# Optimization experiments

Measured on AMD Instinct MI355X. Metric: run time of the kernel, lower is better.

## Reference

```python
import jax, jax.numpy as jnp
import numpy as np

NUM_EXPERTS = 64
TOP_K = 2


def setup_inputs() -> dict:
    key = jax.random.key(0)
    k1, k2 = jax.random.split(key)
    B, D, E = 16384, 4096, NUM_EXPERTS
    routing_features = jax.random.normal(k1, (B, D), dtype=jnp.float32)
    # nn.Linear(D, E, bias=False) weight: [E, D], kaiming-uniform-ish init
    bound = 1.0 / np.sqrt(D)
    gate_w = jax.random.uniform(k2, (E, D), dtype=jnp.float32, minval=-bound, maxval=bound)
    return {"routing_features": routing_features, "gate_w": gate_w}


def reference(routing_features, gate_w):
    B = routing_features.shape[0]
    E, K = NUM_EXPERTS, TOP_K
    # linear gate (no bias): [B, E]
    logits = jnp.einsum("bd,ed->be", routing_features, gate_w)
    full_probs = jax.nn.softmax(logits, axis=-1)
    top_k_logits, top_k_indices = jax.lax.top_k(logits, K)  # [B, K]
    top_k_weights = jax.nn.softmax(top_k_logits, axis=-1)
    # load-balance loss: f_i = fraction of (token, slot) assignments to expert i
    tokens_per_expert = jnp.zeros((E,), dtype=jnp.float32).at[top_k_indices.reshape(-1)].add(1.0)
    f = tokens_per_expert / (B * K)
    P = full_probs.mean(axis=0)
    aux_loss = E * jnp.sum(f * P)
    return top_k_weights, top_k_indices, aux_loss
```

## Files before the change

kernel.cpp:

```cpp
#include <hip/hip_runtime.h>
#include <math.h>


typedef __attribute__((ext_vector_type(8))) short bf16x8;
typedef __attribute__((ext_vector_type(4))) float f32x4;

constexpr int B_ROWS  = 16384;
constexpr int D_DIM   = 4096;
constexpr int E_EXP   = 64;
constexpr int NTHR    = 512;
constexpr int TM      = 128;
constexpr int KSEG    = 256;
constexpr int NSPLIT  = D_DIM / KSEG;
constexpr int NS      = KSEG / 32;
constexpr int FLAGCAP = 8192;
constexpr float GAPTHR = 1e-3f;

__device__ __forceinline__ float wave_max64(float v) {
#pragma unroll
  for (int m = 32; m >= 1; m >>= 1) v = fmaxf(v, __shfl_xor(v, m, 64));
  return v;
}
__device__ __forceinline__ float wave_sum64(float v) {
#pragma unroll
  for (int m = 32; m >= 1; m >>= 1) v += __shfl_xor(v, m, 64);
  return v;
}
__device__ __forceinline__ void wave_argmax64(float v, int i, float& mv, int& mi) {
#pragma unroll
  for (int m = 32; m >= 1; m >>= 1) {
    float ov = __shfl_xor(v, m, 64);
    int   oi = __shfl_xor(i, m, 64);
    if (ov > v || (ov == v && oi < i)) { v = ov; i = oi; }
  }
  mv = v; mi = i;
}

__device__ __forceinline__ void async_copy16(void* lds_dst, const void* g_src) {
  auto g = (const __attribute__((address_space(1))) char*)(g_src);
  auto l = (__attribute__((address_space(3))) char*)(lds_dst);
  __builtin_amdgcn_global_load_lds(g, l, 16, 0, 0);
}

__device__ __forceinline__ void split8(const f32x4 a, const f32x4 b, bf16x8& hi, bf16x8& lo) {
  float f[8] = {a[0], a[1], a[2], a[3], b[0], b[1], b[2], b[3]};
#pragma unroll
  for (int i = 0; i < 8; ++i) {
    unsigned int u = __float_as_uint(f[i]);
    hi[i] = (short)(u >> 16);
    float rem = f[i] - __uint_as_float(u & 0xffff0000u);
    lo[i] = (short)(__float_as_uint(rem) >> 16);
  }
}

__global__ __launch_bounds__(NTHR) void wsplit(const float* __restrict__ gw,
                                               char* __restrict__ wsW,
                                               unsigned int* __restrict__ hdr) {
  const int n = blockIdx.x;
  const int t = threadIdx.x;
  if (n == 0 && t < 192) hdr[t] = 0u;
  const int lane = t & 63, h = (t >> 6) & 1, wc = t >> 7;
  const int col = wc * 16 + (lane & 15);
  const int k0  = n * 32 + (lane >> 4) * 8;
  const float* src = gw + (size_t)col * D_DIM + k0;
  union { unsigned short us[8]; uint4 v; } pk;
#pragma unroll
  for (int i = 0; i < 8; ++i) {
    float f = src[i];
    unsigned int u = __float_as_uint(f);
    if (h == 0) {
      pk.us[i] = (unsigned short)(u >> 16);
    } else {
      float rem = f - __uint_as_float(u & 0xffff0000u);
      pk.us[i] = (unsigned short)(__float_as_uint(rem) >> 16);
    }
  }
  *(uint4*)(wsW + (size_t)n * 8192 + (size_t)t * 16) = pk.v;
}

__global__ __launch_bounds__(NTHR) void gemm_partial(
    const float* __restrict__ rf, const char* __restrict__ wsW,
    float* __restrict__ part) {
  __shared__ char wlds[NS * 8192] __attribute__((aligned(16)));

  const int t = threadIdx.x, lane = t & 63, wv = t >> 6;
  const int ks   = blockIdx.x >> 7;
  const int rb   = blockIdx.x & 127;
  const int row0 = rb * TM;

  {
    const char* src = wsW + (size_t)ks * (NS * 8192);
#pragma unroll
    for (int i = 0; i < NS; ++i)
      async_copy16(wlds + i * 8192 + t * 16, src + i * 8192 + t * 16);
  }
  __syncthreads();

  const float* aptr = rf + (size_t)(row0 + wv * 16 + (lane & 15)) * D_DIM
                         + ks * KSEG + (lane >> 4) * 8;

  f32x4 acc[4] = {{0.f,0.f,0.f,0.f},{0.f,0.f,0.f,0.f},{0.f,0.f,0.f,0.f},{0.f,0.f,0.f,0.f}};
  f32x4 a0[4], a1[4];

#define LDA(s, n) { a0[s] = *(const f32x4*)(aptr + (n) * 32); \
                    a1[s] = *(const f32x4*)(aptr + (n) * 32 + 4); }

  LDA(0, 0); LDA(1, 1); LDA(2, 2); LDA(3, 3);
  __builtin_amdgcn_sched_barrier(0);

#pragma unroll
  for (int n = 0; n < NS; ++n) {
    const int s = n & 3;
    bf16x8 ahi, alo;
    split8(a0[s], a1[s], ahi, alo);
    if (n + 4 < NS) LDA(s, n + 4);
    __builtin_amdgcn_sched_barrier(0);
    const char* wn = wlds + n * 8192 + lane * 16;
#pragma unroll
    for (int cb = 0; cb < 4; ++cb) {
      bf16x8 whi = *(const bf16x8*)(wn + cb * 2048);
      bf16x8 wlo = *(const bf16x8*)(wn + cb * 2048 + 1024);
      acc[cb] = __builtin_amdgcn_mfma_f32_16x16x32_bf16(ahi, whi, acc[cb], 0, 0, 0);
      acc[cb] = __builtin_amdgcn_mfma_f32_16x16x32_bf16(alo, whi, acc[cb], 0, 0, 0);
      acc[cb] = __builtin_amdgcn_mfma_f32_16x16x32_bf16(ahi, wlo, acc[cb], 0, 0, 0);
    }
    __builtin_amdgcn_sched_barrier(0);
  }
#undef LDA

  const int colb = lane & 15;
  const int rowb = (lane >> 4) * 4;
  float* dst = part + ((size_t)ks * B_ROWS + row0 + wv * 16 + rowb) * E_EXP + colb;
#pragma unroll
  for (int cb = 0; cb < 4; ++cb)
#pragma unroll
    for (int j = 0; j < 4; ++j)
      dst[(size_t)j * E_EXP + cb * 16] = acc[cb][j];
}

__global__ __launch_bounds__(NTHR) void epilogue(
    const float* __restrict__ part, float* __restrict__ out,
    float* __restrict__ psum, unsigned int* __restrict__ cnt,
    int* __restrict__ flagcnt, int* __restrict__ flaglist) {
  __shared__ float pcol[E_EXP];
  __shared__ unsigned int scnt[E_EXP];

  const int t = threadIdx.x, lane = t & 63, wv = t >> 6;
  const int row0 = blockIdx.x * 64;

  if (t < E_EXP) { scnt[t] = 0; pcol[t] = 0.f; }
  __syncthreads();

#pragma unroll
  for (int j = 0; j < 8; ++j) {
    const int row = row0 + wv * 8 + j;
    float lg = 0.f;
#pragma unroll
    for (int s = 0; s < NSPLIT; ++s)
      lg += part[((size_t)s * B_ROWS + row) * E_EXP + lane];

    const float m  = wave_max64(lg);
    const float p  = __expf(lg - m);
    const float ss = wave_sum64(p);
    atomicAdd(&pcol[lane], p / ss);

    float v1; int i1; wave_argmax64(lg, lane, v1, i1);
    const float lm1 = (lane == i1) ? -INFINITY : lg;
    float v2; int i2; wave_argmax64(lm1, lane, v2, i2);
    const float lm2 = (lane == i2) ? -INFINITY : lm1;
    float v3; int i3; wave_argmax64(lm2, lane, v3, i3);
    if (lane == 0) {
      const float ex = expf(v2 - v1);
      out[row * 2 + 0] = 1.f / (1.f + ex);
      out[row * 2 + 1] = ex / (1.f + ex);
      out[2 * B_ROWS + row * 2 + 0] = (float)i1;
      out[2 * B_ROWS + row * 2 + 1] = (float)i2;
      atomicAdd(&scnt[i1], 1u);
      atomicAdd(&scnt[i2], 1u);
      if (v1 - v2 < GAPTHR || v2 - v3 < GAPTHR) {
        int fi = atomicAdd(flagcnt, 1);
        if (fi < FLAGCAP) flaglist[fi] = row;
      }
    }
  }
  __syncthreads();
  if (t < E_EXP) {
    atomicAdd(&psum[t], pcol[t]);
    const unsigned int c = scnt[t];
    if (c) atomicAdd(&cnt[t], c);
  }
}

__global__ __launch_bounds__(256) void cleanup(
    const float* __restrict__ rf, const float* __restrict__ gw,
    const int* __restrict__ flagcnt, const int* __restrict__ flaglist,
    const float* __restrict__ psum, const unsigned int* __restrict__ cnt,
    float* __restrict__ out) {
  __shared__ double sm[256];
  const int t = threadIdx.x;
  if (blockIdx.x == 0 && t < 64) {
    const float f = (float)cnt[t] / (float)(B_ROWS * 2);
    const float P = psum[t] / (float)B_ROWS;
    float v = wave_sum64(f * P);
    if (t == 0) out[4 * B_ROWS] = (float)E_EXP * v;
  }
  const int nf = min(*flagcnt, FLAGCAP);
  for (int fi = blockIdx.x; fi < nf; fi += gridDim.x) {
    const int row = flaglist[fi];
    const int e = t & 63, seg = t >> 6;
    const float* a = rf + (size_t)row * D_DIM + seg * 1024;
    const float* w = gw + (size_t)e * D_DIM + seg * 1024;
    double p0 = 0.0, p1 = 0.0, p2 = 0.0, p3 = 0.0;
    for (int k = 0; k < 1024; k += 4) {
      p0 = fma((double)a[k + 0], (double)w[k + 0], p0);
      p1 = fma((double)a[k + 1], (double)w[k + 1], p1);
      p2 = fma((double)a[k + 2], (double)w[k + 2], p2);
      p3 = fma((double)a[k + 3], (double)w[k + 3], p3);
    }
    sm[t] = (p0 + p1) + (p2 + p3);
    __syncthreads();
    if (t < 64) {
      const double l = sm[t] + sm[64 + t] + sm[128 + t] + sm[192 + t];
      double v = l; int ii = t;
#pragma unroll
      for (int m = 32; m >= 1; m >>= 1) {
        double ov = __shfl_xor(v, m, 64); int oi = __shfl_xor(ii, m, 64);
        if (ov > v || (ov == v && oi < ii)) { v = ov; ii = oi; }
      }
      const double v1 = v; const int i1 = ii;
      const double lm = (t == i1) ? -1e300 : l;
      v = lm; ii = t;
#pragma unroll
      for (int m = 32; m >= 1; m >>= 1) {
        double ov = __shfl_xor(v, m, 64); int oi = __shfl_xor(ii, m, 64);
        if (ov > v || (ov == v && oi < ii)) { v = ov; ii = oi; }
      }
      const double v2 = v; const int i2 = ii;
      if (t == 0) {
        const double ex = exp(v2 - v1);
        out[row * 2 + 0] = (float)(1.0 / (1.0 + ex));
        out[row * 2 + 1] = (float)(ex / (1.0 + ex));
        out[2 * B_ROWS + row * 2 + 0] = (float)i1;
        out[2 * B_ROWS + row * 2 + 1] = (float)i2;
      }
    }
    __syncthreads();
  }
}

extern "C" void kernel_launch(void* const* d_in, const int* in_sizes, int n_in,
                              void* d_out, int out_size, void* d_ws, size_t ws_size,
                              hipStream_t stream) {
  const float* rf = (const float*)d_in[0];
  const float* gw = (const float*)d_in[1];
  float* out = (float*)d_out;
  float* psum = (float*)d_ws;
  unsigned int* cnt = (unsigned int*)((char*)d_ws + 256);
  int* flagcnt = (int*)((char*)d_ws + 512);
  int* flaglist = (int*)((char*)d_ws + 768);
  char* wsW = (char*)d_ws + (1u << 20);
  float* part = (float*)((char*)d_ws + (2u << 20));

  wsplit<<<D_DIM / 32, NTHR, 0, stream>>>(gw, wsW, (unsigned int*)d_ws);
  gemm_partial<<<NSPLIT * (B_ROWS / TM), NTHR, 0, stream>>>(rf, wsW, part);
  epilogue<<<B_ROWS / 64, NTHR, 0, stream>>>(part, out, psum, cnt, flagcnt, flaglist);
  cleanup<<<64, 256, 0, stream>>>(rf, gw, flagcnt, flaglist, psum, cnt, out);
}
```

Measured before the change: 237.2 us.

## Double-buffer A and W tiles through LDS with async copies in split-K GEMM

The gate GEMM now streams both the fp32 activation tile (XOR-swizzled) and the split bf16 weights into double-buffered LDS using async copies, overlapping the next stage's loads with the current MFMA work. The K segment per block doubles and the block shrinks to 256 threads, each wave now computing 32 rows with two accumulator sets. This halves the split-K partial output and epilogue reduction traffic and improves reuse of the weight tiles. In exchange each block does longer serial work and synchronizes twice per step, and the manual vmcnt waits must match the copy counts exactly.

```diff
diff --git a/kernel.cpp b/kernel.cpp
--- a/kernel.cpp
+++ b/kernel.cpp
@@ -9,8 +9,9 @@
 constexpr int D_DIM   = 4096;
 constexpr int E_EXP   = 64;
 constexpr int NTHR    = 512;
+constexpr int GTHR    = 256;
 constexpr int TM      = 128;
-constexpr int KSEG    = 256;
+constexpr int KSEG    = 512;
 constexpr int NSPLIT  = D_DIM / KSEG;
 constexpr int NS      = KSEG / 32;
 constexpr int FLAGCAP = 8192;
@@ -78,64 +79,91 @@
   *(uint4*)(wsW + (size_t)n * 8192 + (size_t)t * 16) = pk.v;
 }
 
-__global__ __launch_bounds__(NTHR) void gemm_partial(
+__global__ __launch_bounds__(GTHR) void gemm_partial(
     const float* __restrict__ rf, const char* __restrict__ wsW,
     float* __restrict__ part) {
-  __shared__ char wlds[NS * 8192] __attribute__((aligned(16)));
+  __shared__ char lds[49152] __attribute__((aligned(16)));
 
   const int t = threadIdx.x, lane = t & 63, wv = t >> 6;
-  const int ks   = blockIdx.x >> 7;
-  const int rb   = blockIdx.x & 127;
+  const int rb = blockIdx.x & 127, ks = blockIdx.x >> 7;
   const int row0 = rb * TM;
 
-  {
-    const char* src = wsW + (size_t)ks * (NS * 8192);
-#pragma unroll
-    for (int i = 0; i < NS; ++i)
-      async_copy16(wlds + i * 8192 + t * 16, src + i * 8192 + t * 16);
-  }
-  __syncthreads();
-
-  const float* aptr = rf + (size_t)(row0 + wv * 16 + (lane & 15)) * D_DIM
-                         + ks * KSEG + (lane >> 4) * 8;
-
-  f32x4 acc[4] = {{0.f,0.f,0.f,0.f},{0.f,0.f,0.f,0.f},{0.f,0.f,0.f,0.f},{0.f,0.f,0.f,0.f}};
-  f32x4 a0[4], a1[4];
-
-#define LDA(s, n) { a0[s] = *(const f32x4*)(aptr + (n) * 32); \
-                    a1[s] = *(const f32x4*)(aptr + (n) * 32 + 4); }
-
-  LDA(0, 0); LDA(1, 1); LDA(2, 2); LDA(3, 3);
-  __builtin_amdgcn_sched_barrier(0);
-
-#pragma unroll
+  int goffA[4];
+#pragma unroll
+  for (int j = 0; j < 4; ++j) {
+    const int q = j * GTHR + t;
+    const int row = q >> 3, sl = q & 7;
+    goffA[j] = (row0 + row) * D_DIM + ks * KSEG + ((sl ^ (row & 7)) << 2);
+  }
+  const char* wsrc = wsW + (size_t)(ks * NS) * 8192;
+
+  const int s0 = (lane >> 4) * 2;
+  const int rr0 = wv * 32 + (lane & 15);
+  const int rr1 = rr0 + 16;
+  const int a00 = rr0 * 128 + ((s0 ^ (rr0 & 7)) << 4);
+  const int a01 = rr0 * 128 + (((s0 + 1) ^ (rr0 & 7)) << 4);
+  const int a10 = rr1 * 128 + ((s0 ^ (rr1 & 7)) << 4);
+  const int a11 = rr1 * 128 + (((s0 + 1) ^ (rr1 & 7)) << 4);
+
+  f32x4 acc0[4] = {{0.f,0.f,0.f,0.f},{0.f,0.f,0.f,0.f},{0.f,0.f,0.f,0.f},{0.f,0.f,0.f,0.f}};
+  f32x4 acc1[4] = {{0.f,0.f,0.f,0.f},{0.f,0.f,0.f,0.f},{0.f,0.f,0.f,0.f},{0.f,0.f,0.f,0.f}};
+
+#define ISSUE(n)                                                             \
+  {                                                                          \
+    char* ab_ = lds + ((n) & 1) * 16384;                                     \
+    char* wb_ = lds + 32768 + ((n) & 1) * 8192;                              \
+    _Pragma("unroll") for (int j = 0; j < 4; ++j)                            \
+      async_copy16(ab_ + (j * GTHR + t) * 16, rf + goffA[j] + (n) * 32);     \
+    async_copy16(wb_ + t * 16, wsrc + (size_t)(n) * 8192 + t * 16);          \
+    async_copy16(wb_ + (GTHR + t) * 16,                                      \
+                 wsrc + (size_t)(n) * 8192 + (GTHR + t) * 16);               \
+  }
+
+  ISSUE(0);
+#pragma unroll 2
   for (int n = 0; n < NS; ++n) {
-    const int s = n & 3;
-    bf16x8 ahi, alo;
-    split8(a0[s], a1[s], ahi, alo);
-    if (n + 4 < NS) LDA(s, n + 4);
-    __builtin_amdgcn_sched_barrier(0);
-    const char* wn = wlds + n * 8192 + lane * 16;
+    if (n + 1 < NS) {
+      ISSUE(n + 1);
+      asm volatile("s_waitcnt vmcnt(6)" ::: "memory");
+    } else {
+      asm volatile("s_waitcnt vmcnt(0)" ::: "memory");
+    }
+    __builtin_amdgcn_s_barrier();
+
+    const char* ab = lds + (n & 1) * 16384;
+    const char* wb = lds + 32768 + (n & 1) * 8192 + lane * 16;
+    const f32x4 fl0 = *(const f32x4*)(ab + a00);
+    const f32x4 fh0 = *(const f32x4*)(ab + a01);
+    const f32x4 fl1 = *(const f32x4*)(ab + a10);
+    const f32x4 fh1 = *(const f32x4*)(ab + a11);
+    bf16x8 ahi0, alo0, ahi1, alo1;
+    split8(fl0, fh0, ahi0, alo0);
+    split8(fl1, fh1, ahi1, alo1);
 #pragma unroll
     for (int cb = 0; cb < 4; ++cb) {
-      bf16x8 whi = *(const bf16x8*)(wn + cb * 2048);
-      bf16x8 wlo = *(const bf16x8*)(wn + cb * 2048 + 1024);
-      acc[cb] = __builtin_amdgcn_mfma_f32_16x16x32_bf16(ahi, whi, acc[cb], 0, 0, 0);
-      acc[cb] = __builtin_amdgcn_mfma_f32_16x16x32_bf16(alo, whi, acc[cb], 0, 0, 0);
-      acc[cb] = __builtin_amdgcn_mfma_f32_16x16x32_bf16(ahi, wlo, acc[cb], 0, 0, 0);
-    }
-    __builtin_amdgcn_sched_barrier(0);
-  }
-#undef LDA
+      const bf16x8 whi = *(const bf16x8*)(wb + cb * 2048);
+      const bf16x8 wlo = *(const bf16x8*)(wb + cb * 2048 + 1024);
+      acc0[cb] = __builtin_amdgcn_mfma_f32_16x16x32_bf16(ahi0, whi, acc0[cb], 0, 0, 0);
+      acc0[cb] = __builtin_amdgcn_mfma_f32_16x16x32_bf16(alo0, whi, acc0[cb], 0, 0, 0);
+      acc0[cb] = __builtin_amdgcn_mfma_f32_16x16x32_bf16(ahi0, wlo, acc0[cb], 0, 0, 0);
+      acc1[cb] = __builtin_amdgcn_mfma_f32_16x16x32_bf16(ahi1, whi, acc1[cb], 0, 0, 0);
+      acc1[cb] = __builtin_amdgcn_mfma_f32_16x16x32_bf16(alo1, whi, acc1[cb], 0, 0, 0);
+      acc1[cb] = __builtin_amdgcn_mfma_f32_16x16x32_bf16(ahi1, wlo, acc1[cb], 0, 0, 0);
+    }
+    __builtin_amdgcn_s_barrier();
+  }
+#undef ISSUE
 
   const int colb = lane & 15;
   const int rowb = (lane >> 4) * 4;
-  float* dst = part + ((size_t)ks * B_ROWS + row0 + wv * 16 + rowb) * E_EXP + colb;
+  float* dst = part + ((size_t)ks * B_ROWS + row0 + wv * 32 + rowb) * E_EXP + colb;
 #pragma unroll
   for (int cb = 0; cb < 4; ++cb)
 #pragma unroll
-    for (int j = 0; j < 4; ++j)
-      dst[(size_t)j * E_EXP + cb * 16] = acc[cb][j];
+    for (int j = 0; j < 4; ++j) {
+      dst[(size_t)j * E_EXP + cb * 16] = acc0[cb][j];
+      dst[(size_t)(j + 16) * E_EXP + cb * 16] = acc1[cb][j];
+    }
 }
 
 __global__ __launch_bounds__(NTHR) void epilogue(
@@ -262,7 +290,7 @@
   float* part = (float*)((char*)d_ws + (2u << 20));
 
   wsplit<<<D_DIM / 32, NTHR, 0, stream>>>(gw, wsW, (unsigned int*)d_ws);
-  gemm_partial<<<NSPLIT * (B_ROWS / TM), NTHR, 0, stream>>>(rf, wsW, part);
+  gemm_partial<<<NSPLIT * (B_ROWS / TM), GTHR, 0, stream>>>(rf, wsW, part);
   epilogue<<<B_ROWS / 64, NTHR, 0, stream>>>(part, out, psum, cnt, flagcnt, flaglist);
   cleanup<<<64, 256, 0, stream>>>(rf, gw, flagcnt, flaglist, psum, cnt, out);
 }
```

Result: faster. 204.4 us (-13.8%).

## Stage A and W tiles through triple-buffered LDS with async copies

Applied to the files above, without the earlier changes.

The split-K GEMM now uses 256-thread blocks of 64 rows with 512-wide K segments. Each 32-wide K step of both the activation tile (XOR-swizzled) and the split weight tile is loaded asynchronously into a three-slot LDS ring, with vmcnt waits and barriers keeping two stages in flight. Previously activations were loaded straight from global into registers and all the weights were preloaded up front. This aims to overlap global loads with MFMA work and halve the partial-sum traffic, at the cost of more barriers per step and fewer rows per block.

```diff
diff --git a/kernel.cpp b/kernel.cpp
--- a/kernel.cpp
+++ b/kernel.cpp
@@ -9,8 +9,9 @@
 constexpr int D_DIM   = 4096;
 constexpr int E_EXP   = 64;
 constexpr int NTHR    = 512;
-constexpr int TM      = 128;
-constexpr int KSEG    = 256;
+constexpr int GTHR    = 256;
+constexpr int TM      = 64;
+constexpr int KSEG    = 512;
 constexpr int NSPLIT  = D_DIM / KSEG;
 constexpr int NS      = KSEG / 32;
 constexpr int FLAGCAP = 8192;
@@ -78,55 +79,72 @@
   *(uint4*)(wsW + (size_t)n * 8192 + (size_t)t * 16) = pk.v;
 }
 
-__global__ __launch_bounds__(NTHR) void gemm_partial(
+__global__ __launch_bounds__(GTHR) void gemm_partial(
     const float* __restrict__ rf, const char* __restrict__ wsW,
     float* __restrict__ part) {
-  __shared__ char wlds[NS * 8192] __attribute__((aligned(16)));
+  __shared__ char lds[3 * 16384] __attribute__((aligned(16)));
 
   const int t = threadIdx.x, lane = t & 63, wv = t >> 6;
-  const int ks   = blockIdx.x >> 7;
-  const int rb   = blockIdx.x & 127;
+  const int rb = blockIdx.x & 255, ks = blockIdx.x >> 8;
   const int row0 = rb * TM;
 
-  {
-    const char* src = wsW + (size_t)ks * (NS * 8192);
-#pragma unroll
-    for (int i = 0; i < NS; ++i)
-      async_copy16(wlds + i * 8192 + t * 16, src + i * 8192 + t * 16);
-  }
-  __syncthreads();
-
-  const float* aptr = rf + (size_t)(row0 + wv * 16 + (lane & 15)) * D_DIM
-                         + ks * KSEG + (lane >> 4) * 8;
+  int goffA[2];
+#pragma unroll
+  for (int j = 0; j < 2; ++j) {
+    const int q = j * GTHR + t;
+    const int row = q >> 3, sl = q & 7;
+    goffA[j] = (row0 + row) * D_DIM + ks * KSEG + ((sl ^ (row & 7)) << 2);
+  }
+  const char* wsrc = wsW + (size_t)(ks * NS) * 8192;
+
+  const int rr  = wv * 16 + (lane & 15);
+  const int s0  = (lane >> 4) * 2;
+  const int a00 = rr * 128 + ((s0 ^ (rr & 7)) << 4);
+  const int a01 = rr * 128 + (((s0 + 1) ^ (rr & 7)) << 4);
 
   f32x4 acc[4] = {{0.f,0.f,0.f,0.f},{0.f,0.f,0.f,0.f},{0.f,0.f,0.f,0.f},{0.f,0.f,0.f,0.f}};
-  f32x4 a0[4], a1[4];
-
-#define LDA(s, n) { a0[s] = *(const f32x4*)(aptr + (n) * 32); \
-                    a1[s] = *(const f32x4*)(aptr + (n) * 32 + 4); }
-
-  LDA(0, 0); LDA(1, 1); LDA(2, 2); LDA(3, 3);
-  __builtin_amdgcn_sched_barrier(0);
-
+
+#define ISSUE(nn)                                                            \
+  {                                                                          \
+    char* b_ = lds + ((nn) % 3) * 16384;                                     \
+    async_copy16(b_ + t * 16, rf + goffA[0] + (nn) * 32);                    \
+    async_copy16(b_ + (GTHR + t) * 16, rf + goffA[1] + (nn) * 32);           \
+    async_copy16(b_ + 8192 + t * 16, wsrc + (size_t)(nn) * 8192 + t * 16);   \
+    async_copy16(b_ + 8192 + (GTHR + t) * 16,                                \
+                 wsrc + (size_t)(nn) * 8192 + (GTHR + t) * 16);              \
+  }
+
+  ISSUE(0);
+  ISSUE(1);
 #pragma unroll
   for (int n = 0; n < NS; ++n) {
-    const int s = n & 3;
+    if (n + 2 < NS) {
+      ISSUE(n + 2);
+      asm volatile("s_waitcnt vmcnt(8)" ::: "memory");
+    } else if (n + 1 < NS) {
+      asm volatile("s_waitcnt vmcnt(4)" ::: "memory");
+    } else {
+      asm volatile("s_waitcnt vmcnt(0)" ::: "memory");
+    }
+    __builtin_amdgcn_s_barrier();
+
+    const char* ab = lds + (n % 3) * 16384;
+    const char* wb = ab + 8192 + lane * 16;
+    const f32x4 fl = *(const f32x4*)(ab + a00);
+    const f32x4 fh = *(const f32x4*)(ab + a01);
     bf16x8 ahi, alo;
-    split8(a0[s], a1[s], ahi, alo);
-    if (n + 4 < NS) LDA(s, n + 4);
-    __builtin_amdgcn_sched_barrier(0);
-    const char* wn = wlds + n * 8192 + lane * 16;
+    split8(fl, fh, ahi, alo);
 #pragma unroll
     for (int cb = 0; cb < 4; ++cb) {
-      bf16x8 whi = *(const bf16x8*)(wn + cb * 2048);
-      bf16x8 wlo = *(const bf16x8*)(wn + cb * 2048 + 1024);
+      const bf16x8 whi = *(const bf16x8*)(wb + cb * 2048);
+      const bf16x8 wlo = *(const bf16x8*)(wb + cb * 2048 + 1024);
       acc[cb] = __builtin_amdgcn_mfma_f32_16x16x32_bf16(ahi, whi, acc[cb], 0, 0, 0);
       acc[cb] = __builtin_amdgcn_mfma_f32_16x16x32_bf16(alo, whi, acc[cb], 0, 0, 0);
       acc[cb] = __builtin_amdgcn_mfma_f32_16x16x32_bf16(ahi, wlo, acc[cb], 0, 0, 0);
     }
-    __builtin_amdgcn_sched_barrier(0);
-  }
-#undef LDA
+    __builtin_amdgcn_s_barrier();
+  }
+#undef ISSUE
 
   const int colb = lane & 15;
   const int rowb = (lane >> 4) * 4;
@@ -262,7 +280,7 @@
   float* part = (float*)((char*)d_ws + (2u << 20));
 
   wsplit<<<D_DIM / 32, NTHR, 0, stream>>>(gw, wsW, (unsigned int*)d_ws);
-  gemm_partial<<<NSPLIT * (B_ROWS / TM), NTHR, 0, stream>>>(rf, wsW, part);
+  gemm_partial<<<NSPLIT * (B_ROWS / TM), GTHR, 0, stream>>>(rf, wsW, part);
   epilogue<<<B_ROWS / 64, NTHR, 0, stream>>>(part, out, psum, cnt, flagcnt, flaglist);
   cleanup<<<64, 256, 0, stream>>>(rf, gw, flagcnt, flaglist, psum, cnt, out);
 }
```

New measurement: 210.4 us. 11.3% less time.

## Fuse split-K GEMM and epilogue into single-wave full-K router kernel

Applied to the files above, without the earlier changes.

Replaces the split-K GEMM plus separate epilogue with one kernel where each 64-thread block computes full-K logits for 32 rows. A and W tiles are streamed into a 4-slot LDS ring via async copies with manual vmcnt waits, using an XOR swizzle for A. The softmax, top-k and aux statistics are computed in the same kernel from an LDS tile. This removes the partial-sum buffer write and re-read (16 splits × B×E floats) and one kernel launch. The cost is that each block has only one wave, so latency hiding depends on the async prefetch depth and occupancy, and the weights are re-read from L2 by every block.

```diff
diff --git a/kernel.cpp b/kernel.cpp
--- a/kernel.cpp
+++ b/kernel.cpp
@@ -9,10 +9,9 @@
 constexpr int D_DIM   = 4096;
 constexpr int E_EXP   = 64;
 constexpr int NTHR    = 512;
-constexpr int TM      = 128;
-constexpr int KSEG    = 256;
-constexpr int NSPLIT  = D_DIM / KSEG;
-constexpr int NS      = KSEG / 32;
+constexpr int RPB     = 32;
+constexpr int NS      = 128;
+constexpr int SLOT    = 12288;
 constexpr int FLAGCAP = 8192;
 constexpr float GAPTHR = 1e-3f;
 
@@ -59,10 +58,10 @@
   const int n = blockIdx.x;
   const int t = threadIdx.x;
   if (n == 0 && t < 192) hdr[t] = 0u;
-  const int lane = t & 63, h = (t >> 6) & 1, wc = t >> 7;
-  const int col = wc * 16 + (lane & 15);
-  const int k0  = n * 32 + (lane >> 4) * 8;
-  const float* src = gw + (size_t)col * D_DIM + k0;
+  const int lane = t & 63, h = (t >> 6) & 1, er = t >> 7;
+  const int e  = er * 16 + (lane & 15);
+  const int k0 = n * 32 + (lane >> 4) * 8;
+  const float* src = gw + (size_t)e * D_DIM + k0;
   union { unsigned short us[8]; uint4 v; } pk;
 #pragma unroll
   for (int i = 0; i < 8; ++i) {
@@ -78,117 +77,131 @@
   *(uint4*)(wsW + (size_t)n * 8192 + (size_t)t * 16) = pk.v;
 }
 
-__global__ __launch_bounds__(NTHR) void gemm_partial(
+__global__ __launch_bounds__(64) void gemm_router(
     const float* __restrict__ rf, const char* __restrict__ wsW,
-    float* __restrict__ part) {
-  __shared__ char wlds[NS * 8192] __attribute__((aligned(16)));
-
-  const int t = threadIdx.x, lane = t & 63, wv = t >> 6;
-  const int ks   = blockIdx.x >> 7;
-  const int rb   = blockIdx.x & 127;
-  const int row0 = rb * TM;
-
-  {
-    const char* src = wsW + (size_t)ks * (NS * 8192);
-#pragma unroll
-    for (int i = 0; i < NS; ++i)
-      async_copy16(wlds + i * 8192 + t * 16, src + i * 8192 + t * 16);
-  }
-  __syncthreads();
-
-  const float* aptr = rf + (size_t)(row0 + wv * 16 + (lane & 15)) * D_DIM
-                         + ks * KSEG + (lane >> 4) * 8;
-
-  f32x4 acc[4] = {{0.f,0.f,0.f,0.f},{0.f,0.f,0.f,0.f},{0.f,0.f,0.f,0.f},{0.f,0.f,0.f,0.f}};
-  f32x4 a0[4], a1[4];
-
-#define LDA(s, n) { a0[s] = *(const f32x4*)(aptr + (n) * 32); \
-                    a1[s] = *(const f32x4*)(aptr + (n) * 32 + 4); }
-
-  LDA(0, 0); LDA(1, 1); LDA(2, 2); LDA(3, 3);
-  __builtin_amdgcn_sched_barrier(0);
-
-#pragma unroll
-  for (int n = 0; n < NS; ++n) {
-    const int s = n & 3;
-    bf16x8 ahi, alo;
-    split8(a0[s], a1[s], ahi, alo);
-    if (n + 4 < NS) LDA(s, n + 4);
+    float* __restrict__ out, float* __restrict__ psum,
+    unsigned int* __restrict__ cnt, int* __restrict__ flagcnt,
+    int* __restrict__ flaglist) {
+  __shared__ char lds[4 * SLOT] __attribute__((aligned(16)));
+
+  const int lane = threadIdx.x;
+  const int row0 = blockIdx.x * RPB;
+
+  int goffA[4];
+#pragma unroll
+  for (int j = 0; j < 4; ++j) {
+    const int row = 8 * j + (lane >> 3);
+    const int sl  = lane & 7;
+    goffA[j] = (row0 + row) * D_DIM + ((sl ^ (row & 7)) << 2);
+  }
+
+  const int s0 = (lane >> 4) * 2;
+  int aoff[2][2];
+#pragma unroll
+  for (int rr = 0; rr < 2; ++rr) {
+    const int R = 16 * rr + (lane & 15);
+    aoff[rr][0] = R * 128 + (((s0)     ^ (R & 7)) << 4);
+    aoff[rr][1] = R * 128 + (((s0 + 1) ^ (R & 7)) << 4);
+  }
+
+  f32x4 acc[8] = {{0.f,0.f,0.f,0.f},{0.f,0.f,0.f,0.f},{0.f,0.f,0.f,0.f},{0.f,0.f,0.f,0.f},
+                  {0.f,0.f,0.f,0.f},{0.f,0.f,0.f,0.f},{0.f,0.f,0.f,0.f},{0.f,0.f,0.f,0.f}};
+
+#define ISSUE(nn)                                                             \
+  {                                                                           \
+    char* b_ = lds + ((nn) & 3) * SLOT;                                       \
+    _Pragma("unroll") for (int j = 0; j < 4; ++j)                             \
+      async_copy16(b_ + (j * 64 + lane) * 16, rf + goffA[j] + (nn) * 32);     \
+    _Pragma("unroll") for (int j = 0; j < 8; ++j)                             \
+      async_copy16(b_ + 4096 + (j * 64 + lane) * 16,                          \
+                   wsW + (size_t)(nn) * 8192 + (j * 64 + lane) * 16);         \
+  }
+
+#define STEP(nn)                                                              \
+  {                                                                           \
+    const char* ab = lds + ((nn) & 3) * SLOT;                                 \
+    bf16x8 bhi0, blo0, bhi1, blo1;                                            \
+    {                                                                         \
+      f32x4 fl = *(const f32x4*)(ab + aoff[0][0]);                            \
+      f32x4 fh = *(const f32x4*)(ab + aoff[0][1]);                            \
+      split8(fl, fh, bhi0, blo0);                                             \
+    }                                                                         \
+    {                                                                         \
+      f32x4 fl = *(const f32x4*)(ab + aoff[1][0]);                            \
+      f32x4 fh = *(const f32x4*)(ab + aoff[1][1]);                            \
+      split8(fl, fh, bhi1, blo1);                                             \
+    }                                                                         \
+    _Pragma("unroll") for (int er = 0; er < 4; ++er) {                        \
+      const bf16x8 whi = *(const bf16x8*)(ab + 4096 + er * 2048 + lane * 16); \
+      const bf16x8 wlo = *(const bf16x8*)(ab + 4096 + er * 2048 + 1024 + lane * 16); \
+      acc[er*2+0] = __builtin_amdgcn_mfma_f32_16x16x32_bf16(whi, bhi0, acc[er*2+0], 0, 0, 0); \
+      acc[er*2+0] = __builtin_amdgcn_mfma_f32_16x16x32_bf16(wlo, bhi0, acc[er*2+0], 0, 0, 0); \
+      acc[er*2+0] = __builtin_amdgcn_mfma_f32_16x16x32_bf16(whi, blo0, acc[er*2+0], 0, 0, 0); \
+      acc[er*2+1] = __builtin_amdgcn_mfma_f32_16x16x32_bf16(whi, bhi1, acc[er*2+1], 0, 0, 0); \
+      acc[er*2+1] = __builtin_amdgcn_mfma_f32_16x16x32_bf16(wlo, bhi1, acc[er*2+1], 0, 0, 0); \
+      acc[er*2+1] = __builtin_amdgcn_mfma_f32_16x16x32_bf16(whi, blo1, acc[er*2+1], 0, 0, 0); \
+    }                                                                         \
+  }
+
+  ISSUE(0); ISSUE(1); ISSUE(2);
+  for (int n = 0; n < NS - 3; ++n) {
+    asm volatile("s_waitcnt vmcnt(24)" ::: "memory");
     __builtin_amdgcn_sched_barrier(0);
-    const char* wn = wlds + n * 8192 + lane * 16;
-#pragma unroll
-    for (int cb = 0; cb < 4; ++cb) {
-      bf16x8 whi = *(const bf16x8*)(wn + cb * 2048);
-      bf16x8 wlo = *(const bf16x8*)(wn + cb * 2048 + 1024);
-      acc[cb] = __builtin_amdgcn_mfma_f32_16x16x32_bf16(ahi, whi, acc[cb], 0, 0, 0);
-      acc[cb] = __builtin_amdgcn_mfma_f32_16x16x32_bf16(alo, whi, acc[cb], 0, 0, 0);
-      acc[cb] = __builtin_amdgcn_mfma_f32_16x16x32_bf16(ahi, wlo, acc[cb], 0, 0, 0);
-    }
-    __builtin_amdgcn_sched_barrier(0);
-  }
-#undef LDA
-
-  const int colb = lane & 15;
-  const int rowb = (lane >> 4) * 4;
-  float* dst = part + ((size_t)ks * B_ROWS + row0 + wv * 16 + rowb) * E_EXP + colb;
-#pragma unroll
-  for (int cb = 0; cb < 4; ++cb)
-#pragma unroll
-    for (int j = 0; j < 4; ++j)
-      dst[(size_t)j * E_EXP + cb * 16] = acc[cb][j];
-}
-
-__global__ __launch_bounds__(NTHR) void epilogue(
-    const float* __restrict__ part, float* __restrict__ out,
-    float* __restrict__ psum, unsigned int* __restrict__ cnt,
-    int* __restrict__ flagcnt, int* __restrict__ flaglist) {
-  __shared__ float pcol[E_EXP];
-  __shared__ unsigned int scnt[E_EXP];
-
-  const int t = threadIdx.x, lane = t & 63, wv = t >> 6;
-  const int row0 = blockIdx.x * 64;
-
-  if (t < E_EXP) { scnt[t] = 0; pcol[t] = 0.f; }
-  __syncthreads();
-
-#pragma unroll
-  for (int j = 0; j < 8; ++j) {
-    const int row = row0 + wv * 8 + j;
-    float lg = 0.f;
-#pragma unroll
-    for (int s = 0; s < NSPLIT; ++s)
-      lg += part[((size_t)s * B_ROWS + row) * E_EXP + lane];
-
+    STEP(n);
+    ISSUE(n + 3);
+  }
+  asm volatile("s_waitcnt vmcnt(24)" ::: "memory");
+  __builtin_amdgcn_sched_barrier(0);
+  STEP(NS - 3);
+  asm volatile("s_waitcnt vmcnt(12)" ::: "memory");
+  __builtin_amdgcn_sched_barrier(0);
+  STEP(NS - 2);
+  asm volatile("s_waitcnt vmcnt(0)" ::: "memory");
+  __builtin_amdgcn_sched_barrier(0);
+  STEP(NS - 1);
+#undef ISSUE
+#undef STEP
+
+  asm volatile("s_waitcnt vmcnt(0) lgkmcnt(0)" ::: "memory");
+  __builtin_amdgcn_sched_barrier(0);
+  float* lt = (float*)lds;
+#pragma unroll
+  for (int er = 0; er < 4; ++er)
+#pragma unroll
+    for (int rr = 0; rr < 2; ++rr)
+#pragma unroll
+      for (int j = 0; j < 4; ++j)
+        lt[(16 * rr + (lane & 15)) * 65 + 16 * er + (lane >> 4) * 4 + j] = acc[er * 2 + rr][j];
+
+  float Pacc = 0.f;
+  int myCnt = 0;
+  for (int r = 0; r < RPB; ++r) {
+    const float lg = lt[r * 65 + lane];
     const float m  = wave_max64(lg);
     const float p  = __expf(lg - m);
     const float ss = wave_sum64(p);
-    atomicAdd(&pcol[lane], p / ss);
-
+    Pacc += p / ss;
     float v1; int i1; wave_argmax64(lg, lane, v1, i1);
     const float lm1 = (lane == i1) ? -INFINITY : lg;
     float v2; int i2; wave_argmax64(lm1, lane, v2, i2);
     const float lm2 = (lane == i2) ? -INFINITY : lm1;
     float v3; int i3; wave_argmax64(lm2, lane, v3, i3);
+    myCnt += (lane == i1) + (lane == i2);
     if (lane == 0) {
       const float ex = expf(v2 - v1);
+      const int row = row0 + r;
       out[row * 2 + 0] = 1.f / (1.f + ex);
       out[row * 2 + 1] = ex / (1.f + ex);
       out[2 * B_ROWS + row * 2 + 0] = (float)i1;
       out[2 * B_ROWS + row * 2 + 1] = (float)i2;
-      atomicAdd(&scnt[i1], 1u);
-      atomicAdd(&scnt[i2], 1u);
       if (v1 - v2 < GAPTHR || v2 - v3 < GAPTHR) {
         int fi = atomicAdd(flagcnt, 1);
         if (fi < FLAGCAP) flaglist[fi] = row;
       }
     }
   }
-  __syncthreads();
-  if (t < E_EXP) {
-    atomicAdd(&psum[t], pcol[t]);
-    const unsigned int c = scnt[t];
-    if (c) atomicAdd(&cnt[t], c);
-  }
+  atomicAdd(&psum[lane], Pacc);
+  if (myCnt) atomicAdd(&cnt[lane], (unsigned int)myCnt);
 }
 
 __global__ __launch_bounds__(256) void cleanup(
@@ -259,10 +272,9 @@
   int* flagcnt = (int*)((char*)d_ws + 512);
   int* flaglist = (int*)((char*)d_ws + 768);
   char* wsW = (char*)d_ws + (1u << 20);
-  float* part = (float*)((char*)d_ws + (2u << 20));
 
   wsplit<<<D_DIM / 32, NTHR, 0, stream>>>(gw, wsW, (unsigned int*)d_ws);
-  gemm_partial<<<NSPLIT * (B_ROWS / TM), NTHR, 0, stream>>>(rf, wsW, part);
-  epilogue<<<B_ROWS / 64, NTHR, 0, stream>>>(part, out, psum, cnt, flagcnt, flaglist);
+  gemm_router<<<B_ROWS / RPB, 64, 0, stream>>>(rf, wsW, out, psum, cnt,
+                                               flagcnt, flaglist);
   cleanup<<<64, 256, 0, stream>>>(rf, gw, flagcnt, flaglist, psum, cnt, out);
 }
```

New measurement: 257.7 us. 8.6% more time.
